# Optimization experiments

Hardware: AMD Instinct MI355X
Metric: run time of the kernel (lower is better)

The kernel has to match this reference:

```python
import jax, jax.numpy as jnp
import numpy as np

C = 192          # filter_channels (= in_channels in this module)
K = 3            # kernel_size
NB = 10          # num_bins of rational-quadratic spline (VITS default)
TB = 5.0         # tail_bound
NF = 4           # number of ConvFlow steps per branch
L = 3            # DDSConv n_layers
LOG2PI = float(np.log(2.0 * np.pi))


def conv1x1(x, w, b):
    # x: (B, Cin, T), w: (Cout, Cin)
    return jnp.einsum('oi,bit->bot', w, x) + b[None, :, None]


def depthwise(x, w, b, dil):
    # x: (B, C, T), w: (C, 1, K), dilated depthwise conv, 'same' padding
    pad = dil * (K - 1) // 2
    y = jax.lax.conv_general_dilated(
        x, w, window_strides=(1,), padding=[(pad, pad)], rhs_dilation=(dil,),
        dimension_numbers=('NCH', 'OIH', 'NCH'), feature_group_count=x.shape[1])
    return y + b[None, :, None]


def layer_norm_c(x, g, b, eps=1e-5):
    # VITS LayerNorm: normalize over the channel axis (axis=1)
    m = jnp.mean(x, axis=1, keepdims=True)
    v = jnp.mean((x - m) ** 2, axis=1, keepdims=True)
    return (x - m) * jax.lax.rsqrt(v + eps) * g[None, :, None] + b[None, :, None]


def dds(x, x_mask, g, dep_w, dep_b, pw_w, pw_b, ln_g, ln_b):
    # DDSConv: dilated depth-separable conv stack with residual
    if g is not None:
        x = x + g
    for i in range(L):
        dil = K ** i
        y = depthwise(x * x_mask, dep_w[i], dep_b[i], dil)
        y = jax.nn.gelu(layer_norm_c(y, ln_g[i, 0], ln_b[i, 0]))
        y = conv1x1(y, pw_w[i], pw_b[i])
        y = jax.nn.gelu(layer_norm_c(y, ln_g[i, 1], ln_b[i, 1]))
        x = x + y  # dropout disabled in deterministic reference
    return x * x_mask


def ew_affine(z, x_mask, m, logs):
    y = (m[None, :, None] + jnp.exp(logs)[None, :, None] * z) * x_mask
    ld = jnp.sum(logs[None, :, None] * x_mask, axis=(1, 2))
    return y, ld


def rqs_forward(x_in, uw, uh, ud):
    # unconstrained rational-quadratic spline, forward direction, linear tails
    mb = 1e-3  # min bin width / height / derivative
    const = float(np.log(np.expm1(1.0 - mb)))
    inside = (x_in >= -TB) & (x_in <= TB)
    ud = jnp.pad(ud, ((0, 0), (0, 0), (0, 0), (1, 1)), constant_values=const)
    wd = jax.nn.softmax(uw, -1); wd = mb + (1.0 - mb * NB) * wd
    cw = jnp.cumsum(wd, -1)
    cw = jnp.concatenate([jnp.zeros_like(cw[..., :1]), cw], -1)
    cw = 2.0 * TB * cw - TB
    cw = cw.at[..., 0].set(-TB).at[..., -1].set(TB)
    wd = cw[..., 1:] - cw[..., :-1]
    ht = jax.nn.softmax(uh, -1); ht = mb + (1.0 - mb * NB) * ht
    ch = jnp.cumsum(ht, -1)
    ch = jnp.concatenate([jnp.zeros_like(ch[..., :1]), ch], -1)
    ch = 2.0 * TB * ch - TB
    ch = ch.at[..., 0].set(-TB).at[..., -1].set(TB)
    ht = ch[..., 1:] - ch[..., :-1]
    dv = mb + jax.nn.softplus(ud)  # (..., NB+1)
    xc = jnp.clip(x_in, -TB, TB)
    idx = jnp.clip(jnp.sum((xc[..., None] >= cw[..., :-1]).astype(jnp.int32), -1) - 1, 0, NB - 1)
    g = lambda a, i: jnp.take_along_axis(a, i[..., None], -1)[..., 0]
    icw, iw, ich, ih = g(cw, idx), g(wd, idx), g(ch, idx), g(ht, idx)
    idelta = ih / iw
    d0, d1 = g(dv, idx), g(dv, idx + 1)
    th = (xc - icw) / iw
    t1m = th * (1.0 - th)
    den = idelta + (d0 + d1 - 2.0 * idelta) * t1m
    out = ich + ih * (idelta * th * th + d0 * t1m) / den
    dnum = idelta * idelta * (d1 * th * th + 2.0 * idelta * t1m + d0 * (1.0 - th) ** 2)
    lad = jnp.log(dnum) - 2.0 * jnp.log(den)
    return jnp.where(inside, out, x_in), jnp.where(inside, lad, 0.0)


def conv_flow(z, x_mask, g, pre_w, pre_b, dep_w, dep_b, pw_w, pw_b, ln_g, ln_b, proj_w, proj_b):
    x0, x1 = z[:, :1], z[:, 1:]  # (B,1,T) each
    h = conv1x1(x0, pre_w, pre_b)
    h = dds(h, x_mask, g, dep_w, dep_b, pw_w, pw_b, ln_g, ln_b)
    h = conv1x1(h, proj_w, proj_b) * x_mask      # (B, 3*NB-1, T)
    B, _, T = h.shape
    h = h.reshape(B, 1, 3 * NB - 1, T).transpose(0, 1, 3, 2)  # (B,1,T,3*NB-1)
    s = 1.0 / np.sqrt(C)
    x1n, lad = rqs_forward(x1, h[..., :NB] * s, h[..., NB:2 * NB] * s, h[..., 2 * NB:])
    zo = jnp.concatenate([x0, x1n], 1) * x_mask
    return zo, jnp.sum(lad * x_mask, axis=(1, 2))


def _forward(x, x_mask, w, e_q, pre_w, pre_b, proj_w, proj_b,
             dds_dep_w, dds_dep_b, dds_pw_w, dds_pw_b, dds_ln_g, dds_ln_b,
             post_pre_w, post_pre_b, post_proj_w, post_proj_b,
             pdds_dep_w, pdds_dep_b, pdds_pw_w, pdds_pw_b, pdds_ln_g, pdds_ln_b,
             aff_m, aff_logs,
             f_pre_w, f_pre_b, f_dep_w, f_dep_b, f_pw_w, f_pw_b, f_ln_g, f_ln_b, f_proj_w, f_proj_b,
             paff_m, paff_logs,
             p_pre_w, p_pre_b, p_dep_w, p_dep_b, p_pw_w, p_pw_b, p_ln_g, p_ln_b, p_proj_w, p_proj_b):
    x = jax.lax.stop_gradient(x)
    h = conv1x1(x, pre_w, pre_b)
    h = dds(h, x_mask, None, dds_dep_w, dds_dep_b, dds_pw_w, dds_pw_b, dds_ln_g, dds_ln_b)
    h = conv1x1(h, proj_w, proj_b) * x_mask
    hw = conv1x1(w, post_pre_w, post_pre_b)
    hw = dds(hw, x_mask, None, pdds_dep_w, pdds_dep_b, pdds_pw_w, pdds_pw_b, pdds_ln_g, pdds_ln_b)
    hw = conv1x1(hw, post_proj_w, post_proj_b) * x_mask
    e = e_q * x_mask
    zq, ldq = ew_affine(e, x_mask, paff_m, paff_logs)
    gp = h + hw
    for i in range(NF):
        zq, ld = conv_flow(zq, x_mask, gp, p_pre_w[i], p_pre_b[i], p_dep_w[i], p_dep_b[i],
                           p_pw_w[i], p_pw_b[i], p_ln_g[i], p_ln_b[i], p_proj_w[i], p_proj_b[i])
        ldq = ldq + ld
        zq = zq[:, ::-1]  # Flip (logdet 0)
    zu, z1 = zq[:, :1], zq[:, 1:]
    u = jax.nn.sigmoid(zu) * x_mask
    z0 = (w - u) * x_mask
    ldq = ldq + jnp.sum((jax.nn.log_sigmoid(zu) + jax.nn.log_sigmoid(-zu)) * x_mask, axis=(1, 2))
    logq = jnp.sum(-0.5 * (LOG2PI + e * e) * x_mask, axis=(1, 2)) - ldq
    y0 = jnp.log(jnp.maximum(z0, 1e-5)) * x_mask  # Log flow
    ldt = jnp.sum(-y0, axis=(1, 2))
    z = jnp.concatenate([y0, z1], 1)
    z, ld = ew_affine(z, x_mask, aff_m, aff_logs)
    ldt = ldt + ld
    for i in range(NF):
        z, ld = conv_flow(z, x_mask, h, f_pre_w[i], f_pre_b[i], f_dep_w[i], f_dep_b[i],
                          f_pw_w[i], f_pw_b[i], f_ln_g[i], f_ln_b[i], f_proj_w[i], f_proj_b[i])
        ldt = ldt + ld
        z = z[:, ::-1]
    nll = jnp.sum(0.5 * (LOG2PI + z * z) * x_mask, axis=(1, 2)) - ldt
    return nll + logq  # (B,)


def setup_inputs() -> dict:
    key = jax.random.key(0)
    ks = jax.random.split(key, 24)
    B, T = 32, 768
    P = 3 * NB - 1
    r = lambda k, shape, s=0.05: jax.random.normal(k, shape, jnp.float32) * s
    d = {}
    d['x'] = jax.random.normal(ks[0], (B, C, T), jnp.float32)
    d['x_mask'] = jnp.ones((B, 1, T), jnp.float32)
    d['w'] = jax.random.uniform(ks[1], (B, 1, T), jnp.float32) * 10.0 + 1.0  # positive durations
    d['e_q'] = jax.random.normal(ks[2], (B, 2, T), jnp.float32)
    d['pre_w'] = r(ks[3], (C, C)); d['pre_b'] = jnp.zeros((C,), jnp.float32)
    d['proj_w'] = r(ks[4], (C, C)); d['proj_b'] = jnp.zeros((C,), jnp.float32)
    d['dds_dep_w'] = r(ks[5], (L, C, 1, K)); d['dds_dep_b'] = jnp.zeros((L, C), jnp.float32)
    d['dds_pw_w'] = r(ks[6], (L, C, C)); d['dds_pw_b'] = jnp.zeros((L, C), jnp.float32)
    d['dds_ln_g'] = jnp.ones((L, 2, C), jnp.float32); d['dds_ln_b'] = jnp.zeros((L, 2, C), jnp.float32)
    d['post_pre_w'] = r(ks[7], (C, 1)); d['post_pre_b'] = jnp.zeros((C,), jnp.float32)
    d['post_proj_w'] = r(ks[8], (C, C)); d['post_proj_b'] = jnp.zeros((C,), jnp.float32)
    d['pdds_dep_w'] = r(ks[9], (L, C, 1, K)); d['pdds_dep_b'] = jnp.zeros((L, C), jnp.float32)
    d['pdds_pw_w'] = r(ks[10], (L, C, C)); d['pdds_pw_b'] = jnp.zeros((L, C), jnp.float32)
    d['pdds_ln_g'] = jnp.ones((L, 2, C), jnp.float32); d['pdds_ln_b'] = jnp.zeros((L, 2, C), jnp.float32)
    d['aff_m'] = r(ks[11], (2,)); d['aff_logs'] = r(ks[12], (2,))
    d['f_pre_w'] = r(ks[13], (NF, C, 1)); d['f_pre_b'] = jnp.zeros((NF, C), jnp.float32)
    d['f_dep_w'] = r(ks[14], (NF, L, C, 1, K)); d['f_dep_b'] = jnp.zeros((NF, L, C), jnp.float32)
    d['f_pw_w'] = r(ks[15], (NF, L, C, C)); d['f_pw_b'] = jnp.zeros((NF, L, C), jnp.float32)
    d['f_ln_g'] = jnp.ones((NF, L, 2, C), jnp.float32); d['f_ln_b'] = jnp.zeros((NF, L, 2, C), jnp.float32)
    d['f_proj_w'] = r(ks[16], (NF, P, C), 0.01); d['f_proj_b'] = jnp.zeros((NF, P), jnp.float32)
    d['paff_m'] = r(ks[17], (2,)); d['paff_logs'] = r(ks[18], (2,))
    d['p_pre_w'] = r(ks[19], (NF, C, 1)); d['p_pre_b'] = jnp.zeros((NF, C), jnp.float32)
    d['p_dep_w'] = r(ks[20], (NF, L, C, 1, K)); d['p_dep_b'] = jnp.zeros((NF, L, C), jnp.float32)
    d['p_pw_w'] = r(ks[21], (NF, L, C, C)); d['p_pw_b'] = jnp.zeros((NF, L, C), jnp.float32)
    d['p_ln_g'] = jnp.ones((NF, L, 2, C), jnp.float32); d['p_ln_b'] = jnp.zeros((NF, L, 2, C), jnp.float32)
    d['p_proj_w'] = r(ks[22], (NF, P, C), 0.01); d['p_proj_b'] = jnp.zeros((NF, P), jnp.float32)
    return d


def reference(x, x_mask, w, e_q, pre_w, pre_b, proj_w, proj_b,
              dds_dep_w, dds_dep_b, dds_pw_w, dds_pw_b, dds_ln_g, dds_ln_b,
              post_pre_w, post_pre_b, post_proj_w, post_proj_b,
              pdds_dep_w, pdds_dep_b, pdds_pw_w, pdds_pw_b, pdds_ln_g, pdds_ln_b,
              aff_m, aff_logs,
              f_pre_w, f_pre_b, f_dep_w, f_dep_b, f_pw_w, f_pw_b, f_ln_g, f_ln_b, f_proj_w, f_proj_b,
              paff_m, paff_logs,
              p_pre_w, p_pre_b, p_dep_w, p_dep_b, p_pw_w, p_pw_b, p_ln_g, p_ln_b, p_proj_w, p_proj_b):
    return _forward(x, x_mask, w, e_q, pre_w, pre_b, proj_w, proj_b,
                    dds_dep_w, dds_dep_b, dds_pw_w, dds_pw_b, dds_ln_g, dds_ln_b,
                    post_pre_w, post_pre_b, post_proj_w, post_proj_b,
                    pdds_dep_w, pdds_dep_b, pdds_pw_w, pdds_pw_b, pdds_ln_g, pdds_ln_b,
                    aff_m, aff_logs,
                    f_pre_w, f_pre_b, f_dep_w, f_dep_b, f_pw_w, f_pw_b, f_ln_g, f_ln_b, f_proj_w, f_proj_b,
                    paff_m, paff_logs,
                    p_pre_w, p_pre_b, p_dep_w, p_dep_b, p_pw_w, p_pw_b, p_ln_g, p_ln_b, p_proj_w, p_proj_b)
```

## Files before the change

kernel.cpp:

```cpp
#include <hip/hip_runtime.h>
#include <math.h>

#define CC 192
#define TTT 768
#define PP 29
#define LOG2PI_F 1.8378770664093453f
#define WSLOT 36864
#define PSW 6144
#define XS 200
#define XSP 200
#define PARL 1728

typedef __attribute__((ext_vector_type(8))) short short8;
typedef __attribute__((ext_vector_type(4))) float floatx4;
typedef __attribute__((ext_vector_type(2))) float float2v;
union Frag { int4 i; short8 s; };

__device__ __forceinline__ float2v fma2(float2v a, float2v b, float2v c){
  return __builtin_elementwise_fma(a, b, c);
}
__device__ __forceinline__ float geluf(float x){
  float u = 1.5957691216057308f * (x + 0.044715f*x*x*x);
  return x * __builtin_amdgcn_rcpf(1.f + __expf(-u));
}
__device__ __forceinline__ float softplus_f(float x){
  return (x > 20.f) ? x : log1pf(__expf(x));
}
__device__ __forceinline__ float logsig_f(float x){
  return -softplus_f(-x);
}
__device__ __forceinline__ unsigned short f2bf(float f){
  unsigned int u = __builtin_bit_cast(unsigned int, f);
  u += 0x7fffu + ((u >> 16) & 1u);
  return (unsigned short)(u >> 16);
}
__device__ __forceinline__ unsigned int packbf2(float a0, float a1){
  return (unsigned int)f2bf(a0) | ((unsigned int)f2bf(a1) << 16);
}
__device__ __forceinline__ void unbf2(unsigned int u, float& lo, float& hi){
  lo = __builtin_bit_cast(float, u << 16);
  hi = __builtin_bit_cast(float, u & 0xffff0000u);
}
__device__ __forceinline__ float2v unbf2v(unsigned int u){
  float2v r;
  r.x = __builtin_bit_cast(float, u << 16);
  r.y = __builtin_bit_cast(float, u & 0xffff0000u);
  return r;
}
__device__ __forceinline__ void unp8(int4 v, float* o){
  unsigned int* p = (unsigned int*)&v;
  unbf2(p[0], o[0], o[1]); unbf2(p[1], o[2], o[3]);
  unbf2(p[2], o[4], o[5]); unbf2(p[3], o[6], o[7]);
}
__device__ __forceinline__ void f4arr(float4 v, float* o){ o[0]=v.x;o[1]=v.y;o[2]=v.z;o[3]=v.w; }
__device__ __forceinline__ float2v pick2(float4 a, float4 b, int p){
  switch(p){
    case 0: return (float2v){a.x, a.y};
    case 1: return (float2v){a.z, a.w};
    case 2: return (float2v){b.x, b.y};
    default: return (float2v){b.z, b.w};
  }
}

__global__ __launch_bounds__(256) void convert_w_k(
    const float* __restrict__ p0, const float* __restrict__ p1,
    const float* __restrict__ p2, const float* __restrict__ p3,
    const float* __restrict__ p4, const float* __restrict__ p5,
    const float* __restrict__ p6, const float* __restrict__ p7,
    const float* __restrict__ p8, unsigned short* __restrict__ Wb){
  int i = blockIdx.x*256 + threadIdx.x;
  const int totalA = 33*WSLOT;
  const int total = totalA + 8*PSW;
  if (i >= total) return;
  if (i < totalA){
    int slot = i / WSLOT, j = i % WSLOT;
    int e = j & 7, lane = (j>>3) & 63, kt = j >> 9;
    int k = kt % 6, tile = kt / 6;
    int co = tile*16 + (lane & 15);
    int kk = k*32 + (lane>>4)*8 + e;
    int r = co*CC + kk;
    const float* src;
    if      (slot == 0) src = p0 + r;
    else if (slot == 1) src = p1 + r;
    else if (slot == 2) src = p2 + r;
    else if (slot < 6)  src = p3 + (size_t)(slot-3)*WSLOT + r;
    else if (slot < 9)  src = p4 + (size_t)(slot-6)*WSLOT + r;
    else if (slot < 21) src = p5 + (size_t)(slot-9)*WSLOT + r;
    else                src = p6 + (size_t)(slot-21)*WSLOT + r;
    Wb[i] = f2bf(*src);
  } else {
    int r2 = i - totalA;
    int ps = r2 / PSW, j = r2 % PSW;
    int e = j & 7, lane = (j>>3) & 63, kt = j >> 9;
    int k = kt % 6, tile = kt / 6;
    int co = tile*16 + (lane & 15); if (co > PP-1) co = PP-1;
    int kk = k*32 + (lane>>4)*8 + e;
    const float* base = (ps < 4) ? (p7 + (size_t)ps*PP*CC) : (p8 + (size_t)(ps-4)*PP*CC);
    Wb[i] = f2bf(base[co*CC + kk]);
  }
}

__global__ __launch_bounds__(256) void pack_par_k(
    const float* __restrict__ dds_dep_w, const float* __restrict__ dds_dep_b,
    const float* __restrict__ dds_ln_g,  const float* __restrict__ dds_ln_b,
    const float* __restrict__ dds_pw_b,
    const float* __restrict__ pdds_dep_w, const float* __restrict__ pdds_dep_b,
    const float* __restrict__ pdds_ln_g,  const float* __restrict__ pdds_ln_b,
    const float* __restrict__ pdds_pw_b,
    const float* __restrict__ p_dep_w, const float* __restrict__ p_dep_b,
    const float* __restrict__ p_ln_g,  const float* __restrict__ p_ln_b,
    const float* __restrict__ p_pw_b,
    const float* __restrict__ f_dep_w, const float* __restrict__ f_dep_b,
    const float* __restrict__ f_ln_g,  const float* __restrict__ f_ln_b,
    const float* __restrict__ f_pw_b,
    float* __restrict__ P){
  int i = blockIdx.x*256 + threadIdx.x;
  const int total = 30*PARL;
  if (i >= total) return;
  int ls = i / PARL, r = i % PARL;
  int arr = r / 192, c = r % 192;
  const float *dep_w, *dep_b, *ln_g, *ln_b, *pw_b;
  int l;
  if (ls < 3){
    l = ls; dep_w = dds_dep_w; dep_b = dds_dep_b; ln_g = dds_ln_g; ln_b = dds_ln_b; pw_b = dds_pw_b;
  } else if (ls < 6){
    l = ls-3; dep_w = pdds_dep_w; dep_b = pdds_dep_b; ln_g = pdds_ln_g; ln_b = pdds_ln_b; pw_b = pdds_pw_b;
  } else if (ls < 18){
    int f = (ls-6)/3; l = (ls-6)%3;
    dep_w = p_dep_w + (size_t)f*3*CC*3; dep_b = p_dep_b + (size_t)f*3*CC;
    ln_g = p_ln_g + (size_t)f*3*2*CC;  ln_b = p_ln_b + (size_t)f*3*2*CC;
    pw_b = p_pw_b + (size_t)f*3*CC;
  } else {
    int f = (ls-18)/3; l = (ls-18)%3;
    dep_w = f_dep_w + (size_t)f*3*CC*3; dep_b = f_dep_b + (size_t)f*3*CC;
    ln_g = f_ln_g + (size_t)f*3*2*CC;  ln_b = f_ln_b + (size_t)f*3*2*CC;
    pw_b = f_pw_b + (size_t)f*3*CC;
  }
  float v;
  if      (arr < 3)  v = dep_w[((size_t)l*CC + c)*3 + arr];
  else if (arr == 3) v = dep_b[(size_t)l*CC + c];
  else if (arr == 4) v = ln_g[((size_t)l*2+0)*CC + c];
  else if (arr == 5) v = ln_b[((size_t)l*2+0)*CC + c];
  else if (arr == 6) v = ln_g[((size_t)l*2+1)*CC + c];
  else if (arr == 7) v = ln_b[((size_t)l*2+1)*CC + c];
  else               v = pw_b[(size_t)l*CC + c];
  P[i] = v;
}

__global__ __launch_bounds__(256) void transpose_x_k(
    const float* __restrict__ x, unsigned short* __restrict__ xT){
  __shared__ unsigned short tile[32*XS];
  int b = blockIdx.y, t0 = blockIdx.x*32, tid = threadIdx.x;
  int tl4 = (tid & 7)*4, cr = tid >> 3;
  #pragma unroll
  for (int rnd=0; rnd<6; rnd++){
    int c = rnd*32 + cr;
    float4 v4 = *(const float4*)(x + ((size_t)b*CC + c)*TTT + t0 + tl4);
    tile[(tl4+0)*XS + c] = f2bf(v4.x);
    tile[(tl4+1)*XS + c] = f2bf(v4.y);
    tile[(tl4+2)*XS + c] = f2bf(v4.z);
    tile[(tl4+3)*XS + c] = f2bf(v4.w);
  }
  __syncthreads();
  #pragma unroll
  for (int k=0;k<3;k++){
    int task = k*256 + tid;
    int row = task/24, cn = task%24;
    *(int4*)(xT + ((size_t)b*TTT + t0 + row)*CC + cn*8) = *(const int4*)&tile[row*XS + cn*8];
  }
}

__global__ __launch_bounds__(256) void conv_cc_k(
    const unsigned short* __restrict__ in, const unsigned short* __restrict__ Wsw,
    const float* __restrict__ bias, const float* __restrict__ mask,
    const unsigned short* __restrict__ addsrc, unsigned short* __restrict__ outb, int mode){
  __shared__ unsigned short bufX[32*XS];
  __shared__ unsigned short bufY[32*XS];
  __shared__ float marr[32];
  int b = blockIdx.y, t0 = blockIdx.x*32, tid = threadIdx.x;
  #pragma unroll
  for (int k=0;k<3;k++){
    int task = k*256 + tid;
    int row = task/24, cn = task%24;
    const unsigned short* src = in + ((size_t)b*TTT + t0 + row)*CC + cn*8;
    *(int4*)&bufX[row*XS + cn*8] = *(const int4*)src;
    if (mode == 2){
      const unsigned short* s2 = addsrc + ((size_t)b*TTT + t0 + row)*CC + cn*8;
      *(int4*)&bufY[row*XS + cn*8] = *(const int4*)s2;
    }
  }
  if (tid >= 128 && tid < 160) marr[tid-128] = mask[(size_t)b*TTT + t0 + (tid-128)];
  __syncthreads();
  int w = tid >> 6, lane = tid & 63;
  int n16 = lane & 15, quad = lane >> 4;
  Frag af[3][6];
  #pragma unroll
  for (int ct=0; ct<3; ct++){
    int tile = w*3 + ct;
    #pragma unroll
    for (int k=0;k<6;k++)
      af[ct][k].i = *(const int4*)(Wsw + ((size_t)(tile*6 + k)*64 + lane)*8);
  }
  floatx4 acc[3][2];
  #pragma unroll
  for (int ct=0;ct<3;ct++)
    #pragma unroll
    for (int tt=0;tt<2;tt++)
      acc[ct][tt] = (floatx4){0.f,0.f,0.f,0.f};
  #pragma unroll
  for (int k=0;k<6;k++){
    Frag bf[2];
    #pragma unroll
    for (int tt=0;tt<2;tt++)
      bf[tt].i = *(const int4*)&bufX[(tt*16+n16)*XS + k*32 + quad*8];
    #pragma unroll
    for (int ct=0;ct<3;ct++)
      #pragma unroll
      for (int tt=0;tt<2;tt++)
        acc[ct][tt] = __builtin_amdgcn_mfma_f32_16x16x32_bf16(af[ct][k].s, bf[tt].s, acc[ct][tt], 0,0,0);
  }
  __syncthreads();
  #pragma unroll
  for (int ct=0;ct<3;ct++){
    int cobase = w*48 + ct*16 + quad*4;
    float4 b4 = *(const float4*)(bias + cobase);
    float ba[4] = {b4.x, b4.y, b4.z, b4.w};
    #pragma unroll
    for (int tt=0;tt<2;tt++){
      int t = tt*16 + n16;
      float mv = (mode >= 1) ? marr[t] : 1.f;
      float av[4] = {0.f,0.f,0.f,0.f};
      if (mode == 2){
        uint2 uy = *(uint2*)&bufY[t*XS + cobase];
        unbf2(uy.x, av[0], av[1]); unbf2(uy.y, av[2], av[3]);
      }
      float hh[4];
      #pragma unroll
      for (int r=0;r<4;r++){
        float v = acc[ct][tt][r] + ba[r];
        if (mode >= 1) v *= mv;
        if (mode == 2) v += av[r];
        hh[r] = v;
      }
      uint2 wv; wv.x = packbf2(hh[0], hh[1]); wv.y = packbf2(hh[2], hh[3]);
      *(uint2*)&bufX[t*XS + cobase] = wv;
    }
  }
  __syncthreads();
  #pragma unroll
  for (int k=0;k<3;k++){
    int task = k*256 + tid;
    int row = task/24, cn = task%24;
    *(int4*)(outb + ((size_t)b*TTT + t0 + row)*CC + cn*8) = *(const int4*)&bufX[row*XS + cn*8];
  }
}

__global__ __launch_bounds__(256,3) void mega_dds_k(
    const unsigned short* __restrict__ in,
    const float* __restrict__ zsrc, int zstride,
    const unsigned short* __restrict__ g,
    unsigned short* __restrict__ outb,
    const float* __restrict__ mask,
    const float* __restrict__ parP,
    const float* __restrict__ pw1, const float* __restrict__ pb1,
    const unsigned short* __restrict__ Wsw,
    int srcmode, int outmode,
    const unsigned short* __restrict__ projW, const float* __restrict__ projB,
    float* __restrict__ z, int zs, float* __restrict__ acco){
  __shared__ unsigned short ping[64*XSP];
  __shared__ float par[2][PARL];
  __shared__ float mrow[64];
  float* pro = par[0];

  int b = blockIdx.y, t0 = blockIdx.x*32, tid = threadIdx.x;
  int ws0 = t0 - 16;
  int w = tid >> 6, lane = tid & 63;
  int n16 = lane & 15, quad = lane >> 4;
  int row = w*16 + n16;
  const float* mkb = mask + (size_t)b*TTT;
  const int dils[3] = {1,3,9};

  if (tid < 64){
    int gt = ws0 + tid;
    bool inr = (gt >= 0) && (gt < TTT);
    int gc = gt < 0 ? 0 : (gt > TTT-1 ? TTT-1 : gt);
    mrow[tid] = inr ? mkb[gc] : 0.f;
  }
  #pragma unroll
  for (int k=0;k<7;k++){
    int i2 = k*256 + tid;
    if (i2 < PARL) par[0][i2] = parP[i2];
  }
  if (srcmode == 0){
    #pragma unroll
    for (int k=0;k<6;k++){
      int task = k*256 + tid;
      int r = task/24, cn = task%24, c0 = cn*8;
      int gt = ws0 + r;
      bool inr = (gt >= 0) && (gt < TTT);
      int gc = gt < 0 ? 0 : (gt > TTT-1 ? TTT-1 : gt);
      float mv = inr ? mkb[gc] : 0.f;
      float hv[8];
      unp8(*(const int4*)(in + ((size_t)b*TTT + gc)*CC + c0), hv);
      int4 pk;
      pk.x = (int)packbf2(hv[0]*mv, hv[1]*mv); pk.y = (int)packbf2(hv[2]*mv, hv[3]*mv);
      pk.z = (int)packbf2(hv[4]*mv, hv[5]*mv); pk.w = (int)packbf2(hv[6]*mv, hv[7]*mv);
      *(int4*)&ping[r*XSP + c0] = pk;
    }
  } else {
    #pragma unroll
    for (int k=0;k<6;k++){
      int task = k*256 + tid;
      int r = task/24, cn = task%24, c0 = cn*8;
      int gt = ws0 + r;
      bool inr = (gt >= 0) && (gt < TTT);
      int gc = gt < 0 ? 0 : (gt > TTT-1 ? TTT-1 : gt);
      float mv = inr ? mkb[gc] : 0.f;
      float zv = inr ? zsrc[(size_t)b*zstride + gc] : 0.f;
      float hv[8];
      if (g){
        unp8(*(const int4*)(g + ((size_t)b*TTT + gc)*CC + c0), hv);
      } else {
        #pragma unroll
        for (int e=0;e<8;e++) hv[e] = 0.f;
      }
      float4 pwa = *(const float4*)(pw1 + c0);
      float4 pwb2 = *(const float4*)(pw1 + c0 + 4);
      float4 pba = *(const float4*)(pb1 + c0);
      float4 pbb2 = *(const float4*)(pb1 + c0 + 4);
      float pwv[8], pbv[8];
      f4arr(pwa, pwv); f4arr(pwb2, pwv+4);
      f4arr(pba, pbv); f4arr(pbb2, pbv+4);
      float ov[8];
      #pragma unroll
      for (int e=0;e<8;e++) ov[e] = (hv[e] + fmaf(pwv[e], zv, pbv[e]))*mv;
      int4 pk;
      pk.x = (int)packbf2(ov[0], ov[1]); pk.y = (int)packbf2(ov[2], ov[3]);
      pk.z = (int)packbf2(ov[4], ov[5]); pk.w = (int)packbf2(ov[6], ov[7]);
      *(int4*)&ping[r*XSP + c0] = pk;
    }
  }
  __syncthreads();

  #pragma unroll
  for (int l=0; l<3; l++){
    const int dil = dils[l];
    const bool active = (l < 2) || (w == 1) || (w == 2);
    const float* pl = par[l & 1];
    const unsigned short* WL = Wsw + (size_t)l*WSLOT;
    Frag bfr[6];
    Frag afb[2][6];
    floatx4 acc[12];
    if (active){
      int iL = row - dil; iL = iL < 0 ? 0 : iL;
      int iR = row + dil; iR = iR > 63 ? 63 : iR;
      float2v vv[24];
      float2v s2v = {0.f,0.f}, q2v = {0.f,0.f};
      #pragma unroll
      for (int j=0;j<6;j++){
        int kk = j*32 + quad*8;
        int4 L4 = *(const int4*)&ping[iL*XSP + kk];
        int4 C4 = *(const int4*)&ping[row*XSP + kk];
        int4 R4 = *(const int4*)&ping[iR*XSP + kk];
        unsigned int* Lp = (unsigned int*)&L4;
        unsigned int* Cp = (unsigned int*)&C4;
        unsigned int* Rp = (unsigned int*)&R4;
        float4 w0a = *(const float4*)&pl[kk],       w0b = *(const float4*)&pl[kk+4];
        float4 w1a = *(const float4*)&pl[192+kk],   w1b = *(const float4*)&pl[192+kk+4];
        float4 w2a = *(const float4*)&pl[384+kk],   w2b = *(const float4*)&pl[384+kk+4];
        float4 dba = *(const float4*)&pl[576+kk],   dbb = *(const float4*)&pl[576+kk+4];
        #pragma unroll
        for (int p=0;p<4;p++){
          float2v val = fma2(pick2(w0a,w0b,p), unbf2v(Lp[p]),
                        fma2(pick2(w1a,w1b,p), unbf2v(Cp[p]),
                        fma2(pick2(w2a,w2b,p), unbf2v(Rp[p]), pick2(dba,dbb,p))));
          vv[j*4+p] = val;
          s2v += val;
          q2v = fma2(val, val, q2v);
        }
      }
      float s = s2v.x + s2v.y, q = q2v.x + q2v.y;
      s += __shfl_xor(s, 16); s += __shfl_xor(s, 32);
      q += __shfl_xor(q, 16); q += __shfl_xor(q, 32);
      float mm = s*(1.f/CC);
      float rr = rsqrtf(q*(1.f/CC) - mm*mm + 1e-5f);
      {
        float2v mm2 = {mm,mm}, rr2 = {rr,rr};
        #pragma unroll
        for (int j=0;j<6;j++){
          int kk = j*32 + quad*8;
          float4 g0a = *(const float4*)&pl[768+kk], g0b = *(const float4*)&pl[768+kk+4];
          float4 b0a = *(const float4*)&pl[960+kk], b0b = *(const float4*)&pl[960+kk+4];
          unsigned int wwp[4];
          #pragma unroll
          for (int p=0;p<4;p++){
            float2v a = fma2((vv[j*4+p]-mm2)*rr2, pick2(g0a,g0b,p), pick2(b0a,b0b,p));
            wwp[p] = packbf2(geluf(a.x), geluf(a.y));
          }
          bfr[j].i = make_int4((int)wwp[0], (int)wwp[1], (int)wwp[2], (int)wwp[3]);
        }
      }
      #pragma unroll
      for (int k=0;k<6;k++)
        afb[0][k].i = *(const int4*)(WL + ((size_t)(0*6 + k)*64 + lane)*8);
      #pragma unroll
      for (int k=0;k<6;k++)
        afb[1][k].i = *(const int4*)(WL + ((size_t)(1*6 + k)*64 + lane)*8);
    }
    __syncthreads();
    if (l < 2){
      const float* src = parP + (size_t)(l+1)*PARL;
      #pragma unroll
      for (int k=0;k<7;k++){
        int i2 = k*256 + tid;
        if (i2 < PARL) par[(l+1)&1][i2] = src[i2];
      }
    }
    if (active){
      #pragma unroll
      for (int tile=0; tile<12; tile++){
        int cur = tile & 1;
        acc[tile] = (floatx4){0.f,0.f,0.f,0.f};
        #pragma unroll
        for (int k=0;k<6;k++)
          acc[tile] = __builtin_amdgcn_mfma_f32_16x16x32_bf16(afb[cur][k].s, bfr[k].s, acc[tile], 0,0,0);
        if (tile < 10){
          #pragma unroll
          for (int k=0;k<6;k++)
            afb[cur][k].i = *(const int4*)(WL + ((size_t)((tile+2)*6 + k)*64 + lane)*8);
        }
      }
      float2v s2p = {0.f,0.f}, q2p = {0.f,0.f};
      #pragma unroll
      for (int tile=0; tile<12; tile++){
        int co = tile*16 + quad*4;
        float4 pbv = *(const float4*)&pl[1536+co];
        acc[tile][0] += pbv.x; acc[tile][1] += pbv.y;
        acc[tile][2] += pbv.z; acc[tile][3] += pbv.w;
        float2v v01 = {acc[tile][0], acc[tile][1]};
        float2v v23 = {acc[tile][2], acc[tile][3]};
        s2p += v01 + v23;
        q2p = fma2(v01, v01, q2p);
        q2p = fma2(v23, v23, q2p);
      }
      float s2 = s2p.x + s2p.y, q2 = q2p.x + q2p.y;
      s2 += __shfl_xor(s2, 16); s2 += __shfl_xor(s2, 32);
      q2 += __shfl_xor(q2, 16); q2 += __shfl_xor(q2, 32);
      float cmP = s2*(1.f/CC);
      float crP = rsqrtf(q2*(1.f/CC) - cmP*cmP + 1e-5f);
      float mc = mrow[row];
      float2v mc2 = {mc,mc};
      float2v cm2 = {cmP,cmP}, cr2 = {crP,crP};
      #pragma unroll
      for (int tile=0; tile<12; tile++){
        int co = tile*16 + quad*4;
        float4 g1v = *(const float4*)&pl[1152+co];
        float4 b1v = *(const float4*)&pl[1344+co];
        uint2 ux = *(uint2*)&ping[row*XSP + co];
        float2v x01 = unbf2v(ux.x), x23 = unbf2v(ux.y);
        float2v v01 = {acc[tile][0], acc[tile][1]};
        float2v v23 = {acc[tile][2], acc[tile][3]};
        float2v a01 = fma2((v01-cm2)*cr2, (float2v){g1v.x,g1v.y}, (float2v){b1v.x,b1v.y});
        float2v a23 = fma2((v23-cm2)*cr2, (float2v){g1v.z,g1v.w}, (float2v){b1v.z,b1v.w});
        float2v h01 = (x01 + (float2v){geluf(a01.x), geluf(a01.y)}) * mc2;
        float2v h23 = (x23 + (float2v){geluf(a23.x), geluf(a23.y)}) * mc2;
        uint2 wv;
        wv.x = packbf2(h01.x, h01.y);
        wv.y = packbf2(h23.x, h23.y);
        *(uint2*)&ping[row*XSP + co] = wv;
      }
    }
    __syncthreads();
  }

  if (outmode == 0){
    #pragma unroll
    for (int k=0;k<3;k++){
      int task = k*256 + tid;
      int r = task/24, cn = task%24, c0 = cn*8;
      *(int4*)(outb + ((size_t)b*TTT + t0 + r)*CC + c0) = *(const int4*)&ping[(16+r)*XSP + c0];
    }
    return;
  }

  {
    int rowg = w >> 1, ctp = w & 1;
    int prow = 16 + rowg*16 + n16;
    Frag afp[6];
    #pragma unroll
    for (int k=0;k<6;k++)
      afp[k].i = *(const int4*)(projW + ((size_t)(ctp*6 + k)*64 + lane)*8);
    Frag bfp[6];
    #pragma unroll
    for (int k=0;k<6;k++)
      bfp[k].i = *(const int4*)&ping[prow*XSP + k*32 + quad*8];
    floatx4 acc2 = (floatx4){0.f,0.f,0.f,0.f};
    #pragma unroll
    for (int k=0;k<6;k++)
      acc2 = __builtin_amdgcn_mfma_f32_16x16x32_bf16(afp[k].s, bfp[k].s, acc2, 0,0,0);
    int rt = prow - 16;
    float mv = mrow[prow];
    #pragma unroll
    for (int r=0;r<4;r++){
      int co = ctp*16 + quad*4 + r;
      if (co < PP) pro[rt*30 + co] = (acc2[r] + projB[co]) * mv;
    }
  }
  __syncthreads();
  if (tid < 32){
    const float scv = 0.07216878364870323f;
    int tg = t0 + tid;
    float m = mrow[16+tid];
    float* z0p = z + ((size_t)b*2 + zs)*TTT + tg;
    float* z1p = z + ((size_t)b*2 + (1-zs))*TTT + tg;
    float xs = *z1p;
    float uw[10], uh[10], ud[9];
    #pragma unroll
    for (int k=0;k<10;k++) uw[k]=pro[tid*30+k]*scv;
    #pragma unroll
    for (int k=0;k<10;k++) uh[k]=pro[tid*30+10+k]*scv;
    #pragma unroll
    for (int k=0;k<9;k++)  ud[k]=pro[tid*30+20+k];
    bool inside = (xs >= -5.f) && (xs <= 5.f);
    float xc = fminf(fmaxf(xs,-5.f),5.f);
    float mx=uw[0];
    #pragma unroll
    for (int k=1;k<10;k++) mx=fmaxf(mx,uw[k]);
    float sw=0.f; float wd[10];
    #pragma unroll
    for (int k=0;k<10;k++){ wd[k]=__expf(uw[k]-mx); sw+=wd[k]; }
    float invw = 1.f/sw;
    #pragma unroll
    for (int k=0;k<10;k++) wd[k]=fmaf(0.99f*invw, wd[k], 1e-3f);
    float mh=uh[0];
    #pragma unroll
    for (int k=1;k<10;k++) mh=fmaxf(mh,uh[k]);
    float sh=0.f; float ht[10];
    #pragma unroll
    for (int k=0;k<10;k++){ ht[k]=__expf(uh[k]-mh); sh+=ht[k]; }
    float invh = 1.f/sh;
    #pragma unroll
    for (int k=0;k<10;k++) ht[k]=fmaf(0.99f*invh, ht[k], 1e-3f);
    float cw=-5.f, icw=-5.f, iw=1.f; int idx=0;
    #pragma unroll
    for (int i2=0;i2<10;i2++){
      float nw = (i2==9) ? 5.f : fmaf(10.f, wd[i2], cw);
      if (cw <= xc){ idx=i2; icw=cw; iw=nw-cw; }
      cw=nw;
    }
    float ch=-5.f, ich=-5.f, ih=1.f;
    #pragma unroll
    for (int i2=0;i2<10;i2++){
      float nh = (i2==9) ? 5.f : fmaf(10.f, ht[i2], ch);
      if (i2==idx){ ich=ch; ih=nh-ch; }
      ch=nh;
    }
    const float UDC = logf(expm1f(0.999f));
    float d0=1.f, d1=1.f;
    #pragma unroll
    for (int k=0;k<11;k++){
      float uu = (k==0 || k==10) ? UDC : ud[k-1];
      float dk = 1e-3f + softplus_f(uu);
      if (k==idx)   d0=dk;
      if (k==idx+1) d1=dk;
    }
    float idel = ih/iw;
    float th = (xc-icw)/iw;
    float t1m = th*(1.f-th);
    float den = idel + (d0+d1-2.f*idel)*t1m;
    float outv = ich + ih*(idel*th*th + d0*t1m)/den;
    float omt = 1.f-th;
    float dnum = idel*idel*(d1*th*th + 2.f*idel*t1m + d0*omt*omt);
    float lad = logf(dnum) - 2.f*logf(den);
    float y = inside ? outv : xs;
    lad = inside ? lad : 0.f;
    *z1p = y*m;
    *z0p = (*z0p)*m;
    float lm = lad*m;
    lm += __shfl_xor(lm, 1); lm += __shfl_xor(lm, 2);
    lm += __shfl_xor(lm, 4); lm += __shfl_xor(lm, 8);
    lm += __shfl_xor(lm, 16);
    if (tid == 0) atomicAdd(acco + b, -lm);
  }
}

__global__ __launch_bounds__(256) void init_z_k(
    const float* __restrict__ e_q, const float* __restrict__ mask,
    const float* __restrict__ pm, const float* __restrict__ pl,
    float* __restrict__ z, float* __restrict__ acc){
  __shared__ float red[256];
  int b = blockIdx.y; int t = blockIdx.x*256 + threadIdx.x;
  float m = mask[(size_t)b*TTT + t];
  float pl0=pl[0], pl1=pl[1];
  float e0 = e_q[((size_t)b*2+0)*TTT + t]*m;
  float e1 = e_q[((size_t)b*2+1)*TTT + t]*m;
  z[((size_t)b*2+0)*TTT + t] = fmaf(__expf(pl0), e0, pm[0])*m;
  z[((size_t)b*2+1)*TTT + t] = fmaf(__expf(pl1), e1, pm[1])*m;
  float contrib = -0.5f*(LOG2PI_F + e0*e0)*m - 0.5f*(LOG2PI_F + e1*e1)*m - (pl0+pl1)*m;
  int tid = threadIdx.x;
  red[tid] = contrib;
  __syncthreads();
  for (int o=128;o>0;o>>=1){ if (tid<o) red[tid]+=red[tid+o]; __syncthreads(); }
  if (tid==0) atomicAdd(acc+b, red[0]);
}

__global__ __launch_bounds__(256) void final_pre_k(
    float* __restrict__ z, const float* __restrict__ w_in, const float* __restrict__ mask,
    const float* __restrict__ am, const float* __restrict__ al, float* __restrict__ acc){
  __shared__ float red[256];
  int b = blockIdx.y; int t = blockIdx.x*256 + threadIdx.x;
  float m = mask[(size_t)b*TTT + t];
  float zu  = z[((size_t)b*2+0)*TTT + t];
  float z1v = z[((size_t)b*2+1)*TTT + t];
  float wv  = w_in[(size_t)b*TTT + t];
  float u  = m / (1.f + __expf(-zu));
  float z0 = (wv - u)*m;
  float y0 = logf(fmaxf(z0, 1e-5f))*m;
  float al0=al[0], al1=al[1];
  z[((size_t)b*2+0)*TTT + t] = fmaf(__expf(al0), y0,  am[0])*m;
  z[((size_t)b*2+1)*TTT + t] = fmaf(__expf(al1), z1v, am[1])*m;
  float contrib = -(logsig_f(zu)+logsig_f(-zu))*m + y0 - (al0+al1)*m;
  int tid = threadIdx.x;
  red[tid] = contrib;
  __syncthreads();
  for (int o=128;o>0;o>>=1){ if (tid<o) red[tid]+=red[tid+o]; __syncthreads(); }
  if (tid==0) atomicAdd(acc+b, red[0]);
}

__global__ __launch_bounds__(256) void final_post_k(
    const float* __restrict__ z, const float* __restrict__ mask, float* __restrict__ acc){
  __shared__ float red[256];
  int b = blockIdx.y; int t = blockIdx.x*256 + threadIdx.x;
  float m = mask[(size_t)b*TTT + t];
  float z0 = z[((size_t)b*2+0)*TTT + t];
  float z1 = z[((size_t)b*2+1)*TTT + t];
  float contrib = 0.5f*(LOG2PI_F + z0*z0)*m + 0.5f*(LOG2PI_F + z1*z1)*m;
  int tid = threadIdx.x;
  red[tid] = contrib;
  __syncthreads();
  for (int o=128;o>0;o>>=1){ if (tid<o) red[tid]+=red[tid+o]; __syncthreads(); }
  if (tid==0) atomicAdd(acc+b, red[0]);
}

__global__ void write_out_k(const float* __restrict__ acc, float* __restrict__ out, int n){
  int i = threadIdx.x;
  if (i < n) out[i] = acc[i];
}

extern "C" void kernel_launch(void* const* d_in, const int* in_sizes, int n_in,
                              void* d_out, int out_size, void* d_ws, size_t ws_size,
                              hipStream_t stream){
  (void)n_in; (void)out_size; (void)ws_size;
  const float* x         = (const float*)d_in[0];
  const float* mask      = (const float*)d_in[1];
  const float* w_in      = (const float*)d_in[2];
  const float* e_q       = (const float*)d_in[3];
  const float* pre_w     = (const float*)d_in[4];
  const float* pre_b     = (const float*)d_in[5];
  const float* proj_w    = (const float*)d_in[6];
  const float* proj_b    = (const float*)d_in[7];
  const float* dds_dep_w = (const float*)d_in[8];
  const float* dds_dep_b = (const float*)d_in[9];
  const float* dds_pw_w  = (const float*)d_in[10];
  const float* dds_pw_b  = (const float*)d_in[11];
  const float* dds_ln_g  = (const float*)d_in[12];
  const float* dds_ln_b  = (const float*)d_in[13];
  const float* post_pre_w  = (const float*)d_in[14];
  const float* post_pre_b  = (const float*)d_in[15];
  const float* post_proj_w = (const float*)d_in[16];
  const float* post_proj_b = (const float*)d_in[17];
  const float* pdds_dep_w  = (const float*)d_in[18];
  const float* pdds_dep_b  = (const float*)d_in[19];
  const float* pdds_pw_w   = (const float*)d_in[20];
  const float* pdds_pw_b   = (const float*)d_in[21];
  const float* pdds_ln_g   = (const float*)d_in[22];
  const float* pdds_ln_b   = (const float*)d_in[23];
  const float* aff_m    = (const float*)d_in[24];
  const float* aff_logs = (const float*)d_in[25];
  const float* f_pre_w  = (const float*)d_in[26];
  const float* f_pre_b  = (const float*)d_in[27];
  const float* f_dep_w  = (const float*)d_in[28];
  const float* f_dep_b  = (const float*)d_in[29];
  const float* f_pw_w   = (const float*)d_in[30];
  const float* f_pw_b   = (const float*)d_in[31];
  const float* f_ln_g   = (const float*)d_in[32];
  const float* f_ln_b   = (const float*)d_in[33];
  const float* f_proj_w = (const float*)d_in[34];
  const float* f_proj_b = (const float*)d_in[35];
  const float* paff_m    = (const float*)d_in[36];
  const float* paff_logs = (const float*)d_in[37];
  const float* p_pre_w  = (const float*)d_in[38];
  const float* p_pre_b  = (const float*)d_in[39];
  const float* p_dep_w  = (const float*)d_in[40];
  const float* p_dep_b  = (const float*)d_in[41];
  const float* p_pw_w   = (const float*)d_in[42];
  const float* p_pw_b   = (const float*)d_in[43];
  const float* p_ln_g   = (const float*)d_in[44];
  const float* p_ln_b   = (const float*)d_in[45];
  const float* p_proj_w = (const float*)d_in[46];
  const float* p_proj_b = (const float*)d_in[47];

  int Bn = in_sizes[0] / (CC*TTT);
  size_t big2 = (size_t)Bn*CC*TTT;
  unsigned short* xT = (unsigned short*)d_ws;
  unsigned short* A  = xT + big2;
  unsigned short* Bb = A  + big2;
  unsigned short* H  = Bb + big2;
  unsigned short* GP = H  + big2;
  unsigned short* Wb = GP + big2;
  size_t wtot = 33*(size_t)WSLOT + 8*(size_t)PSW;
  float* parP = (float*)(Wb + ((wtot + 7) & ~(size_t)7));
  float* zbuf = parP + 30*(size_t)PARL;
  float* acc  = zbuf + (size_t)Bn*2*TTT;

  hipMemsetAsync(acc, 0, Bn*sizeof(float), stream);
  convert_w_k<<<(int)((wtot + 255)/256), 256, 0, stream>>>(
      pre_w, proj_w, post_proj_w, dds_pw_w, pdds_pw_w, p_pw_w, f_pw_w,
      p_proj_w, f_proj_w, Wb);
  pack_par_k<<<(30*PARL + 255)/256, 256, 0, stream>>>(
      dds_dep_w, dds_dep_b, dds_ln_g, dds_ln_b, dds_pw_b,
      pdds_dep_w, pdds_dep_b, pdds_ln_g, pdds_ln_b, pdds_pw_b,
      p_dep_w, p_dep_b, p_ln_g, p_ln_b, p_pw_b,
      f_dep_w, f_dep_b, f_ln_g, f_ln_b, f_pw_b, parP);

  dim3 g32(TTT/32, Bn), g256(TTT/256, Bn);
  dim3 b256(256);

  unsigned short* W_pre      = Wb + 0*(size_t)WSLOT;
  unsigned short* W_proj     = Wb + 1*(size_t)WSLOT;
  unsigned short* W_postproj = Wb + 2*(size_t)WSLOT;
  unsigned short* W_dds      = Wb + 3*(size_t)WSLOT;
  unsigned short* W_pdds     = Wb + 6*(size_t)WSLOT;
  unsigned short* W_ppw      = Wb + 9*(size_t)WSLOT;
  unsigned short* W_fpw      = Wb + 21*(size_t)WSLOT;
  unsigned short* W_pproj    = Wb + 33*(size_t)WSLOT;
  unsigned short* W_fproj    = W_pproj + 4*(size_t)PSW;

  transpose_x_k<<<g32, b256, 0, stream>>>(x, xT);

  conv_cc_k<<<g32, b256, 0, stream>>>(xT, W_pre, pre_b, mask, nullptr, A, 0);
  mega_dds_k<<<g32, b256, 0, stream>>>(A, nullptr, 0, nullptr, Bb, mask,
      parP + 0*(size_t)3*PARL, nullptr, nullptr,
      W_dds, 0, 0, nullptr, nullptr, nullptr, 0, acc);
  conv_cc_k<<<g32, b256, 0, stream>>>(Bb, W_proj, proj_b, mask, nullptr, H, 1);

  mega_dds_k<<<g32, b256, 0, stream>>>(nullptr, w_in, TTT, nullptr, A, mask,
      parP + 1*(size_t)3*PARL, post_pre_w, post_pre_b,
      W_pdds, 1, 0, nullptr, nullptr, nullptr, 0, acc);
  conv_cc_k<<<g32, b256, 0, stream>>>(A, W_postproj, post_proj_b, mask, H, GP, 2);

  init_z_k<<<g256, b256, 0, stream>>>(e_q, mask, paff_m, paff_logs, zbuf, acc);

  for (int f=0; f<4; f++){
    int s = f & 1;
    mega_dds_k<<<g32, b256, 0, stream>>>(nullptr, zbuf + (size_t)s*TTT, 2*TTT, GP, nullptr, mask,
        parP + (size_t)(2+f)*3*PARL,
        p_pre_w + (size_t)f*CC, p_pre_b + (size_t)f*CC,
        W_ppw + (size_t)f*3*WSLOT, 1, 1,
        W_pproj + (size_t)f*PSW, p_proj_b + (size_t)f*PP, zbuf, s, acc);
  }

  final_pre_k<<<g256, b256, 0, stream>>>(zbuf, w_in, mask, aff_m, aff_logs, acc);

  for (int f=0; f<4; f++){
    int s = f & 1;
    mega_dds_k<<<g32, b256, 0, stream>>>(nullptr, zbuf + (size_t)s*TTT, 2*TTT, H, nullptr, mask,
        parP + (size_t)(6+f)*3*PARL,
        f_pre_w + (size_t)f*CC, f_pre_b + (size_t)f*CC,
        W_fpw + (size_t)f*3*WSLOT, 1, 1,
        W_fproj + (size_t)f*PSW, f_proj_b + (size_t)f*PP, zbuf, s, acc);
  }

  final_post_k<<<g256, b256, 0, stream>>>(zbuf, mask, acc);
  write_out_k<<<1, 64, 0, stream>>>(acc, (float*)d_out, Bn);
}
```

Before: 838.3 us.

## Split last DDS layer output channels across all four waves

In the third DDS layer only two of the four waves did work (the 32 center rows). Now all four waves participate: each pair of waves covers the same 16 rows, and each wave computes half of the 192 output channels (6 tiles). The layer-norm partial sums are exchanged through a small shared array with an extra barrier. The weight-fragment prefetch is also changed from a two-tile-ahead preload to a one-tile-ahead double buffer issued before each tile's MFMAs. The cost is an extra __syncthreads and redundant depthwise/LN1 work per wave in the last layer.

New measurement: 2.259 ms. 2.69x slower.

```diff
diff --git a/kernel.cpp b/kernel.cpp
--- a/kernel.cpp
+++ b/kernel.cpp
@@ -270,6 +270,7 @@
   __shared__ unsigned short ping[64*XSP];
   __shared__ float par[2][PARL];
   __shared__ float mrow[64];
+  __shared__ float sqx[32][2][2];
   float* pro = par[0];
 
   int b = blockIdx.y, t0 = blockIdx.x*32, tid = threadIdx.x;
@@ -345,22 +346,22 @@
   #pragma unroll
   for (int l=0; l<3; l++){
     const int dil = dils[l];
-    const bool active = (l < 2) || (w == 1) || (w == 2);
+    const int NT = (l==2) ? 6 : 12;
+    const int tb = (l==2) ? ((w&1)*6) : 0;
+    const int rowL = (l==2) ? (16 + (w>>1)*16 + n16) : row;
     const float* pl = par[l & 1];
-    const unsigned short* WL = Wsw + (size_t)l*WSLOT;
     Frag bfr[6];
-    Frag afb[2][6];
     floatx4 acc[12];
-    if (active){
-      int iL = row - dil; iL = iL < 0 ? 0 : iL;
-      int iR = row + dil; iR = iR > 63 ? 63 : iR;
+    {
+      int iL = rowL - dil; iL = iL < 0 ? 0 : iL;
+      int iR = rowL + dil; iR = iR > 63 ? 63 : iR;
       float2v vv[24];
       float2v s2v = {0.f,0.f}, q2v = {0.f,0.f};
       #pragma unroll
       for (int j=0;j<6;j++){
         int kk = j*32 + quad*8;
         int4 L4 = *(const int4*)&ping[iL*XSP + kk];
-        int4 C4 = *(const int4*)&ping[row*XSP + kk];
+        int4 C4 = *(const int4*)&ping[rowL*XSP + kk];
         int4 R4 = *(const int4*)&ping[iR*XSP + kk];
         unsigned int* Lp = (unsigned int*)&L4;
         unsigned int* Cp = (unsigned int*)&C4;
@@ -400,12 +401,6 @@
           bfr[j].i = make_int4((int)wwp[0], (int)wwp[1], (int)wwp[2], (int)wwp[3]);
         }
       }
-      #pragma unroll
-      for (int k=0;k<6;k++)
-        afb[0][k].i = *(const int4*)(WL + ((size_t)(0*6 + k)*64 + lane)*8);
-      #pragma unroll
-      for (int k=0;k<6;k++)
-        afb[1][k].i = *(const int4*)(WL + ((size_t)(1*6 + k)*64 + lane)*8);
     }
     __syncthreads();
     if (l < 2){
@@ -416,24 +411,29 @@
         if (i2 < PARL) par[(l+1)&1][i2] = src[i2];
       }
     }
-    if (active){
-      #pragma unroll
-      for (int tile=0; tile<12; tile++){
-        int cur = tile & 1;
+    {
+      const unsigned short* WL = Wsw + (size_t)l*WSLOT;
+      Frag afb[2][6];
+      #pragma unroll
+      for (int k=0;k<6;k++)
+        afb[0][k].i = *(const int4*)(WL + ((size_t)((tb+0)*6 + k)*64 + lane)*8);
+      #pragma unroll
+      for (int tile=0; tile<NT; tile++){
+        int cur = tile & 1, nxt = cur ^ 1;
+        if (tile < NT-1){
+          #pragma unroll
+          for (int k=0;k<6;k++)
+            afb[nxt][k].i = *(const int4*)(WL + ((size_t)((tb+tile+1)*6 + k)*64 + lane)*8);
+        }
         acc[tile] = (floatx4){0.f,0.f,0.f,0.f};
         #pragma unroll
         for (int k=0;k<6;k++)
           acc[tile] = __builtin_amdgcn_mfma_f32_16x16x32_bf16(afb[cur][k].s, bfr[k].s, acc[tile], 0,0,0);
-        if (tile < 10){
-          #pragma unroll
-          for (int k=0;k<6;k++)
-            afb[cur][k].i = *(const int4*)(WL + ((size_t)((tile+2)*6 + k)*64 + lane)*8);
-        }
       }
       float2v s2p = {0.f,0.f}, q2p = {0.f,0.f};
       #pragma unroll
-      for (int tile=0; tile<12; tile++){
-        int co = tile*16 + quad*4;
+      for (int tile=0; tile<NT; tile++){
+        int co = (tb+tile)*16 + quad*4;
         float4 pbv = *(const float4*)&pl[1536+co];
         acc[tile][0] += pbv.x; acc[tile][1] += pbv.y;
         acc[tile][2] += pbv.z; acc[tile][3] += pbv.w;
@@ -446,17 +446,25 @@
       float s2 = s2p.x + s2p.y, q2 = q2p.x + q2p.y;
       s2 += __shfl_xor(s2, 16); s2 += __shfl_xor(s2, 32);
       q2 += __shfl_xor(q2, 16); q2 += __shfl_xor(q2, 32);
+      if (l == 2){
+        int r16 = rowL - 16;
+        if (quad == 0){ sqx[r16][w&1][0] = s2; sqx[r16][w&1][1] = q2; }
+        __syncthreads();
+        int oh = (w&1)^1;
+        s2 += sqx[r16][oh][0];
+        q2 += sqx[r16][oh][1];
+      }
       float cmP = s2*(1.f/CC);
       float crP = rsqrtf(q2*(1.f/CC) - cmP*cmP + 1e-5f);
-      float mc = mrow[row];
+      float mc = mrow[rowL];
       float2v mc2 = {mc,mc};
       float2v cm2 = {cmP,cmP}, cr2 = {crP,crP};
       #pragma unroll
-      for (int tile=0; tile<12; tile++){
-        int co = tile*16 + quad*4;
+      for (int tile=0; tile<NT; tile++){
+        int co = (tb+tile)*16 + quad*4;
         float4 g1v = *(const float4*)&pl[1152+co];
         float4 b1v = *(const float4*)&pl[1344+co];
-        uint2 ux = *(uint2*)&ping[row*XSP + co];
+        uint2 ux = *(uint2*)&ping[rowL*XSP + co];
         float2v x01 = unbf2v(ux.x), x23 = unbf2v(ux.y);
         float2v v01 = {acc[tile][0], acc[tile][1]};
         float2v v23 = {acc[tile][2], acc[tile][3]};
@@ -467,7 +475,7 @@
         uint2 wv;
         wv.x = packbf2(h01.x, h01.y);
         wv.y = packbf2(h23.x, h23.y);
-        *(uint2*)&ping[row*XSP + co] = wv;
+        *(uint2*)&ping[rowL*XSP + co] = wv;
       }
     }
     __syncthreads();
@@ -484,8 +492,8 @@
   }
 
   {
-    int rowg = w >> 1, ctp = w & 1;
-    int prow = 16 + rowg*16 + n16;
+    int ctp = w & 1;
+    int prow = 16 + (w>>1)*16 + n16;
     Frag afp[6];
     #pragma unroll
     for (int k=0;k<6;k++)
```
